# Kernel tuning notes

Hardware: AMD Instinct MI355X
Metric: run time of the kernel (lower is better)

Reference implementation:

```python
import jax, jax.numpy as jnp
import numpy as np
import math

D_MODEL = 1024
N_HEAD = 16
HEAD_DIM = D_MODEL // N_HEAD
SEQ_LEN = 512
INIT_SIZE = 1568  # from RelativeSinusoidalPositionalEmbedding default


def _rel_pos_embedding(seq_len, embedding_dim):
    # Replicates RelativeSinusoidalPositionalEmbedding with init_size=1568
    num_embeddings = INIT_SIZE + 1  # 1569
    half_dim = embedding_dim // 2
    scale = math.log(10000.0) / (half_dim - 1)
    freqs = np.exp(np.arange(half_dim, dtype=np.float32) * -scale)
    pos = np.arange(-(num_embeddings // 2), num_embeddings // 2, dtype=np.float32)  # [-785, 784)
    emb = pos[:, None] * freqs[None, :]
    weights = np.concatenate([np.sin(emb), np.cos(emb)], axis=1).astype(np.float32)  # (1569, d)
    weights[0, :] = 0.0  # padding_idx
    origin_shift = num_embeddings // 2 + 1  # 785
    positions = np.arange(-seq_len, seq_len) + origin_shift
    embed = weights[positions]  # (2*seq_len, d)
    return jnp.asarray(embed.T)  # (d, 2*seq_len), matching .T in __init__


def setup_inputs() -> dict:
    key = jax.random.key(0)
    k1, k2, k3, k4, k5 = jax.random.split(key, 5)
    x = jax.random.normal(k1, (8, SEQ_LEN, D_MODEL), dtype=jnp.float32)
    prev = jax.random.normal(k2, (8, N_HEAD, SEQ_LEN, SEQ_LEN), dtype=jnp.float32)
    # Linear(d_model, 3*d_model, bias=False): store as (d_model, 3*d_model) for x @ W
    Wqkv = jax.random.normal(k3, (D_MODEL, 3 * D_MODEL), dtype=jnp.float32) / math.sqrt(D_MODEL)
    r_r_bias = jax.random.normal(k4, (1, N_HEAD, 1, HEAD_DIM), dtype=jnp.float32) * 0.02
    r_w_bias = jax.random.normal(k5, (1, N_HEAD, 1, HEAD_DIM), dtype=jnp.float32) * 0.02
    rel_pos = _rel_pos_embedding(SEQ_LEN, HEAD_DIM)  # (head_dim, 2*seq_len)
    return {"x": x, "prev": prev, "Wqkv": Wqkv, "r_r_bias": r_r_bias,
            "r_w_bias": r_w_bias, "rel_pos": rel_pos, "skip_op": 1}


def _shift(BD, seq_len):
    # BD: (b, h, L, 2L) -> (b, h, L, L) via Transformer-XL pad/reshape trick
    b, h, L, two_L = BD.shape
    BD = jnp.pad(BD, ((0, 0), (0, 0), (0, 0), (0, 1)))        # (b,h,L,2L+1)
    BD = BD.reshape(b, h, -1, L)                               # (b,h,2L+1,L)
    BD = BD[:, :, :-1].reshape(b, h, L, -1)                    # (b,h,L,2L)
    return BD[:, :, :, seq_len:]                               # (b,h,L,L)


def reference(x, prev, Wqkv, r_r_bias, r_w_bias, rel_pos, skip_op):
    b, L, d = x.shape
    qkv = x @ Wqkv                                             # (b,L,3d)
    q, k, v = jnp.split(qkv, 3, axis=-1)
    q = q.reshape(b, L, N_HEAD, HEAD_DIM).transpose(0, 2, 1, 3)  # (b,h,L,hd)
    k = k.reshape(b, L, N_HEAD, HEAD_DIM).transpose(0, 2, 1, 3)
    v = v.reshape(b, L, N_HEAD, HEAD_DIM).transpose(0, 2, 1, 3)

    AC = jnp.einsum('bhqd,bhkd->bhqk', q + r_r_bias, k)
    BD = jnp.einsum('bhqd,dp->bhqp', q + r_w_bias, rel_pos)    # (b,h,L,2L)
    BD = _shift(BD, SEQ_LEN)
    E = jnp.einsum('bhkd,dp->bhkp', k, rel_pos)
    E = _shift(E, SEQ_LEN).transpose(0, 1, 3, 2)
    attn_score = (AC + BD + E) / math.sqrt(HEAD_DIM)
    if skip_op:
        attn_score = attn_score + prev
    prev_out = attn_score
    attn = jax.nn.softmax(attn_score, axis=-1)
    out = jnp.einsum('bhqk,bhkd->bhqd', attn, v)
    out = out.transpose(0, 2, 1, 3).reshape(b, L, d)
    return out, prev_out
```

## Files before the change

kernel.cpp:

```cpp
#include <hip/hip_runtime.h>
#include <hip/hip_bf16.h>
#include <math.h>

namespace {
constexpr int Bn = 8;
constexpr int Hn = 16;
constexpr int Ln = 512;
constexpr int HD = 64;
constexpr int DM = 1024;
constexpr int TL = 1024;
constexpr size_t QS  = (size_t)Bn * Hn * Ln * HD;
constexpr size_t FSz = (size_t)Hn * Ln * Ln;
constexpr size_t WN  = (size_t)DM * 3 * DM;
}

typedef __bf16 bf16x8 __attribute__((ext_vector_type(8)));
typedef float f32x4 __attribute__((ext_vector_type(4)));

typedef __attribute__((address_space(1))) void as1_void_t;
typedef __attribute__((address_space(3))) void as3_void_t;

__device__ __forceinline__ void gload_lds16(const void* g, void* l) {
  __builtin_amdgcn_global_load_lds((as1_void_t*)g, (as3_void_t*)l, 16, 0, 0);
}

__device__ __forceinline__ unsigned short f2bf(float f) {
  unsigned int u = __float_as_uint(f);
  u += 0x7fffu + ((u >> 16) & 1u);
  return (unsigned short)(u >> 16);
}
__device__ __forceinline__ float bf2f(unsigned short h) {
  return __uint_as_float(((unsigned int)h) << 16);
}

__global__ __launch_bounds__(256) void conv_x(const float* __restrict__ x,
                                              unsigned short* __restrict__ xh,
                                              unsigned short* __restrict__ xl) {
  size_t i = ((size_t)blockIdx.x * 256 + threadIdx.x) * 4;
  float4 v = *(const float4*)(x + i);
  unsigned short h0 = f2bf(v.x), h1 = f2bf(v.y), h2 = f2bf(v.z), h3 = f2bf(v.w);
  ushort4 hv = make_ushort4(h0, h1, h2, h3);
  ushort4 lv = make_ushort4(f2bf(v.x - bf2f(h0)), f2bf(v.y - bf2f(h1)),
                            f2bf(v.z - bf2f(h2)), f2bf(v.w - bf2f(h3)));
  *(ushort4*)(xh + i) = hv;
  *(ushort4*)(xl + i) = lv;
}

__global__ __launch_bounds__(256) void conv_w(const float* __restrict__ W,
                                              unsigned short* __restrict__ wh,
                                              unsigned short* __restrict__ wl) {
  __shared__ unsigned short Th[64][72];
  __shared__ unsigned short Tl[64][72];
  const int t = threadIdx.x;
  const int n0 = blockIdx.x * 64;
  const int k0 = blockIdx.y * 64;
#pragma unroll
  for (int i = 0; i < 4; ++i) {
    int row = i * 16 + (t >> 4);
    int col = (t & 15) * 4;
    float4 v = *(const float4*)(W + (size_t)(k0 + row) * 3072 + n0 + col);
    unsigned short h;
    h = f2bf(v.x); Th[row][col + 0] = h; Tl[row][col + 0] = f2bf(v.x - bf2f(h));
    h = f2bf(v.y); Th[row][col + 1] = h; Tl[row][col + 1] = f2bf(v.y - bf2f(h));
    h = f2bf(v.z); Th[row][col + 2] = h; Tl[row][col + 2] = f2bf(v.z - bf2f(h));
    h = f2bf(v.w); Th[row][col + 3] = h; Tl[row][col + 3] = f2bf(v.w - bf2f(h));
  }
  __syncthreads();
  const int rn = t & 63, qq = t >> 6;
  unsigned int hw[8], lw[8];
#pragma unroll
  for (int j = 0; j < 8; ++j) {
    unsigned short a = Th[qq * 16 + 2 * j][rn], b = Th[qq * 16 + 2 * j + 1][rn];
    hw[j] = (unsigned int)a | ((unsigned int)b << 16);
    unsigned short c = Tl[qq * 16 + 2 * j][rn], d = Tl[qq * 16 + 2 * j + 1][rn];
    lw[j] = (unsigned int)c | ((unsigned int)d << 16);
  }
  size_t o = (size_t)(n0 + rn) * 1024 + k0 + qq * 16;
  *(uint4*)(wh + o)     = make_uint4(hw[0], hw[1], hw[2], hw[3]);
  *(uint4*)(wh + o + 8) = make_uint4(hw[4], hw[5], hw[6], hw[7]);
  *(uint4*)(wl + o)     = make_uint4(lw[0], lw[1], lw[2], lw[3]);
  *(uint4*)(wl + o + 8) = make_uint4(lw[4], lw[5], lw[6], lw[7]);
}

__global__ __launch_bounds__(256, 2) void qkv_mfma(const unsigned short* __restrict__ xh,
                                                   const unsigned short* __restrict__ xl,
                                                   const unsigned short* __restrict__ wh,
                                                   const unsigned short* __restrict__ wl,
                                                   float* __restrict__ qarr,
                                                   float* __restrict__ karr,
                                                   float* __restrict__ varr) {
  __shared__ alignas(16) unsigned short Ah[128 * 32];
  __shared__ alignas(16) unsigned short Al[128 * 32];
  __shared__ alignas(16) unsigned short Bh[128 * 32];
  __shared__ alignas(16) unsigned short Bl[128 * 32];
  const int t = threadIdx.x;
  const int lane = t & 63;
  const int w = t >> 6;
  const int m0 = blockIdx.y * 128;
  const int n0 = blockIdx.x * 128;
  const int wr = w >> 1, wc = w & 1;
  const int l16 = lane & 15, s = lane >> 4;

  const unsigned short* gsrc = (w == 0) ? xh : (w == 1) ? xl : (w == 2) ? wh : wl;
  unsigned short* lbase = (w == 0) ? Ah : (w == 1) ? Al : (w == 2) ? Bh : Bl;
  const int rbase = (w < 2) ? m0 : n0;
  const int srow = lane >> 2, sc = lane & 3;

  int aoff[4], boff[4];
#pragma unroll
  for (int f = 0; f < 4; ++f) {
    int Rm = wr * 64 + f * 16 + l16;
    aoff[f] = Rm * 64 + ((s ^ ((Rm >> 1) & 3)) << 4);
    int Rn = wc * 64 + f * 16 + l16;
    boff[f] = Rn * 64 + ((s ^ ((Rn >> 1) & 3)) << 4);
  }

  f32x4 acc[4][4];
#pragma unroll
  for (int i = 0; i < 4; ++i)
#pragma unroll
    for (int j = 0; j < 4; ++j) acc[i][j] = (f32x4){0.f, 0.f, 0.f, 0.f};

  const char* Ahc = (const char*)Ah;
  const char* Alc = (const char*)Al;
  const char* Bhc = (const char*)Bh;
  const char* Blc = (const char*)Bl;

  for (int k0 = 0; k0 < 1024; k0 += 32) {
#pragma unroll
    for (int u = 0; u < 8; ++u) {
      int row = u * 16 + srow;
      int chunk = sc ^ ((row >> 1) & 3);
      gload_lds16(gsrc + (size_t)(rbase + row) * 1024 + k0 + chunk * 8,
                  lbase + u * 512);
    }
    __syncthreads();

    bf16x8 a_h[4], a_l[4], b_h[4], b_l[4];
#pragma unroll
    for (int f = 0; f < 4; ++f) {
      a_h[f] = *(const bf16x8*)(Ahc + aoff[f]);
      b_h[f] = *(const bf16x8*)(Bhc + boff[f]);
    }
#pragma unroll
    for (int i = 0; i < 4; ++i)
#pragma unroll
      for (int j = 0; j < 4; ++j)
        acc[i][j] = __builtin_amdgcn_mfma_f32_16x16x32_bf16(a_h[i], b_h[j], acc[i][j], 0, 0, 0);
#pragma unroll
    for (int f = 0; f < 4; ++f) b_l[f] = *(const bf16x8*)(Blc + boff[f]);
#pragma unroll
    for (int i = 0; i < 4; ++i)
#pragma unroll
      for (int j = 0; j < 4; ++j)
        acc[i][j] = __builtin_amdgcn_mfma_f32_16x16x32_bf16(a_h[i], b_l[j], acc[i][j], 0, 0, 0);
#pragma unroll
    for (int f = 0; f < 4; ++f) a_l[f] = *(const bf16x8*)(Alc + aoff[f]);
#pragma unroll
    for (int i = 0; i < 4; ++i)
#pragma unroll
      for (int j = 0; j < 4; ++j)
        acc[i][j] = __builtin_amdgcn_mfma_f32_16x16x32_bf16(a_l[i], b_h[j], acc[i][j], 0, 0, 0);
    __syncthreads();
  }

  const int part = n0 >> 10;
  float* dst = (part == 0) ? qarr : (part == 1 ? karr : varr);
  const int nb = n0 & 1023;
#pragma unroll
  for (int i = 0; i < 4; ++i) {
#pragma unroll
    for (int j = 0; j < 4; ++j) {
      const int n = nb + wc * 64 + j * 16 + l16;
      const int h = n >> 6, d = n & 63;
#pragma unroll
      for (int r = 0; r < 4; ++r) {
        int m = m0 + wr * 64 + i * 16 + (lane >> 4) * 4 + r;
        int bb = m >> 9, l = m & 511;
        dst[(((size_t)(bb * Hn + h) * Ln + l) << 6) + d] = acc[i][j][r];
      }
    }
  }
}

__global__ __launch_bounds__(256) void fg_gemm(const float* __restrict__ qarr,
                                               const float* __restrict__ karr,
                                               const float* __restrict__ rwb,
                                               const float* __restrict__ R,
                                               float* __restrict__ Fs,
                                               float* __restrict__ Gs,
                                               int b) {
  const int m0 = blockIdx.y * 64;
  const int n0 = blockIdx.x * 64;
  if (m0 + n0 + 126 < 512 || m0 + n0 >= 1024) return;

  __shared__ float As[64][68];
  __shared__ float Rs[64][68];
  const int t = threadIdx.x;
  const int h = blockIdx.z >> 1;
  const int which = blockIdx.z & 1;
  const float* A = (which == 0 ? qarr : karr) + (size_t)(b * Hn + h) * Ln * HD;

#pragma unroll
  for (int i = 0; i < 4; ++i) {
    int idx = t + i * 256;
    int r = idx >> 4;
    int c4 = (idx & 15) * 4;
    float4 av = *(const float4*)(A + (size_t)(m0 + r) * HD + c4);
    if (which == 0) {
      float4 bv = *(const float4*)(rwb + h * HD + c4);
      av.x += bv.x; av.y += bv.y; av.z += bv.z; av.w += bv.w;
    }
    As[c4 + 0][r] = av.x; As[c4 + 1][r] = av.y;
    As[c4 + 2][r] = av.z; As[c4 + 3][r] = av.w;
    *(float4*)(&Rs[r][c4]) = *(const float4*)(R + (size_t)r * TL + n0 + c4);
  }
  __syncthreads();
  const int tr = t >> 4, tc = t & 15;
  float acc[4][4];
#pragma unroll
  for (int i = 0; i < 4; ++i)
#pragma unroll
    for (int j = 0; j < 4; ++j) acc[i][j] = 0.f;
#pragma unroll 16
  for (int kk = 0; kk < 64; ++kk) {
    float a[4], bb[4];
    *(float4*)(a)  = *(const float4*)(&As[kk][tr * 4]);
    *(float4*)(bb) = *(const float4*)(&Rs[kk][tc * 4]);
#pragma unroll
    for (int i = 0; i < 4; ++i)
#pragma unroll
      for (int j = 0; j < 4; ++j) acc[i][j] = fmaf(a[i], bb[j], acc[i][j]);
  }
  if (which == 0) {
    float* O = Fs + (size_t)h * Ln * Ln;
#pragma unroll
    for (int i = 0; i < 4; ++i) {
      const int q = m0 + tr * 4 + i;
#pragma unroll
      for (int jj = 0; jj < 4; ++jj) {
        const int p = n0 + tc * 4 + jj;
        const int j = p + q - 512;
        if ((unsigned)j < 512u) O[((size_t)q << 9) + j] = acc[i][jj];
      }
    }
  } else {
    float* O = Gs + (size_t)h * Ln * Ln;
#pragma unroll
    for (int i = 0; i < 4; ++i) {
      const int jrow = m0 + tr * 4 + i;
#pragma unroll
      for (int jj = 0; jj < 4; ++jj) {
        const int p = n0 + tc * 4 + jj;
        const int q = p + jrow - 512;
        if ((unsigned)q < 512u) O[((size_t)q << 9) + jrow] = acc[i][jj];
      }
    }
  }
}

__global__ __launch_bounds__(256) void attn_fused(const float* __restrict__ qarr,
                                                  const float* __restrict__ karr,
                                                  const float* __restrict__ varr,
                                                  const float* __restrict__ rrb,
                                                  const float* __restrict__ Fs,
                                                  const float* __restrict__ Gs,
                                                  const float* __restrict__ prev,
                                                  const int* __restrict__ skip,
                                                  float* __restrict__ out,
                                                  float* __restrict__ pout,
                                                  int b) {
  __shared__ float qrT[64][18];
  __shared__ float ktT[64][68];
  __shared__ float vt[64][68];
  __shared__ float St[16][68];
  __shared__ float red[16][16];
  __shared__ float mrun[16], lrun[16], mnew_s[16], alpha_s[16];

  const int t = threadIdx.x;
  const int h = blockIdx.y;
  const int q0 = blockIdx.x * 16;
  const float pf = (skip[0] != 0) ? 1.f : 0.f;
  const size_t bh = (size_t)(b * Hn + h);

  {
    int r = t >> 4, c4 = (t & 15) * 4;
    float4 av = *(const float4*)(qarr + (bh * Ln + q0 + r) * HD + c4);
    float4 bv = *(const float4*)(rrb + h * HD + c4);
    qrT[c4 + 0][r] = av.x + bv.x; qrT[c4 + 1][r] = av.y + bv.y;
    qrT[c4 + 2][r] = av.z + bv.z; qrT[c4 + 3][r] = av.w + bv.w;
  }
  if (t < 16) { mrun[t] = -INFINITY; lrun[t] = 0.f; }

  const int tq = t >> 4, tj = t & 15;
  const int d = t & 63, qg = t >> 6;
  float O[4] = {0.f, 0.f, 0.f, 0.f};

  for (int jt = 0; jt < 8; ++jt) {
    const int j0 = jt * 64;
    __syncthreads();
#pragma unroll
    for (int i = 0; i < 4; ++i) {
      int idx = t + i * 256;
      int r = idx >> 4, c4 = (idx & 15) * 4;
      float4 kv = *(const float4*)(karr + (bh * Ln + j0 + r) * HD + c4);
      ktT[c4 + 0][r] = kv.x; ktT[c4 + 1][r] = kv.y;
      ktT[c4 + 2][r] = kv.z; ktT[c4 + 3][r] = kv.w;
      *(float4*)(&vt[r][c4]) = *(const float4*)(varr + (bh * Ln + j0 + r) * HD + c4);
    }
    __syncthreads();

    float s[4] = {0.f, 0.f, 0.f, 0.f};
#pragma unroll 8
    for (int dd = 0; dd < 64; ++dd) {
      float a = qrT[dd][tq];
      float4 bv = *(const float4*)(&ktT[dd][tj * 4]);
      s[0] = fmaf(a, bv.x, s[0]);
      s[1] = fmaf(a, bv.y, s[1]);
      s[2] = fmaf(a, bv.z, s[2]);
      s[3] = fmaf(a, bv.w, s[3]);
    }
    {
      const int q = q0 + tq;
      const size_t pbase = ((bh * Ln + q) << 9) + j0 + tj * 4;
      const size_t fbase = (((size_t)h * Ln + q) << 9) + j0 + tj * 4;
      float4 pv4 = *(const float4*)(prev + pbase);
      float4 fv4 = *(const float4*)(Fs + fbase);
      float4 gv4 = *(const float4*)(Gs + fbase);
      const float pin[4] = {pv4.x, pv4.y, pv4.z, pv4.w};
      const float fin[4] = {fv4.x, fv4.y, fv4.z, fv4.w};
      const float gin[4] = {gv4.x, gv4.y, gv4.z, gv4.w};
      float4 o4;
      float* o4p = &o4.x;
#pragma unroll
      for (int ji = 0; ji < 4; ++ji) {
        float sc = (s[ji] + fin[ji] + gin[ji]) * 0.125f + pf * pin[ji];
        o4p[ji] = sc;
        s[ji] = sc;
        St[tq][tj * 4 + ji] = sc;
      }
      *(float4*)(pout + pbase) = o4;
    }
    __syncthreads();
    {
      const int r = t >> 4, seg = t & 15;
      float mx = St[r][seg * 4];
#pragma unroll
      for (int u = 1; u < 4; ++u) mx = fmaxf(mx, St[r][seg * 4 + u]);
      red[r][seg] = mx;
    }
    __syncthreads();
    if (t < 16) {
      float mx = red[t][0];
#pragma unroll
      for (int u = 1; u < 16; ++u) mx = fmaxf(mx, red[t][u]);
      float mn = fmaxf(mrun[t], mx);
      alpha_s[t] = __expf(mrun[t] - mn);
      mnew_s[t] = mn;
      mrun[t] = mn;
    }
    __syncthreads();
    {
      const float mn = mnew_s[tq];
#pragma unroll
      for (int ji = 0; ji < 4; ++ji) St[tq][tj * 4 + ji] = __expf(s[ji] - mn);
    }
    __syncthreads();
    {
      const int r = t >> 4, seg = t & 15;
      float sm = 0.f;
#pragma unroll
      for (int u = 0; u < 4; ++u) sm += St[r][seg * 4 + u];
      red[r][seg] = sm;
    }
    __syncthreads();
    if (t < 16) {
      float sm = 0.f;
#pragma unroll
      for (int u = 0; u < 16; ++u) sm += red[t][u];
      lrun[t] = lrun[t] * alpha_s[t] + sm;
    }
#pragma unroll
    for (int i = 0; i < 4; ++i) O[i] *= alpha_s[qg * 4 + i];
#pragma unroll 8
    for (int j = 0; j < 64; ++j) {
      float vv = vt[j][d];
#pragma unroll
      for (int i = 0; i < 4; ++i) O[i] = fmaf(St[qg * 4 + i][j], vv, O[i]);
    }
  }
  __syncthreads();
#pragma unroll
  for (int i = 0; i < 4; ++i) {
    int lq = qg * 4 + i;
    float val = O[i] / lrun[lq];
    out[((size_t)b * Ln + q0 + lq) * DM + h * HD + d] = val;
  }
}

extern "C" void kernel_launch(void* const* d_in, const int* in_sizes, int n_in,
                              void* d_out, int out_size, void* d_ws, size_t ws_size,
                              hipStream_t stream) {
  const float* x    = (const float*)d_in[0];
  const float* prev = (const float*)d_in[1];
  const float* W    = (const float*)d_in[2];
  const float* rrb  = (const float*)d_in[3];
  const float* rwb  = (const float*)d_in[4];
  const float* R    = (const float*)d_in[5];
  const int*   skip = (const int*)d_in[6];

  float* out  = (float*)d_out;
  float* pout = out + (size_t)Bn * Ln * DM;

  float* ws = (float*)d_ws;
  float* qarr = ws;
  float* karr = ws + QS;
  float* varr = ws + 2 * QS;
  float* Farr = ws + 3 * QS;
  float* Garr = Farr + FSz;

  unsigned short* xh = (unsigned short*)Farr;
  unsigned short* xl = xh + QS;
  unsigned short* wh = xl + QS;
  unsigned short* wl = wh + WN;

  conv_x<<<dim3(4096), 256, 0, stream>>>(x, xh, xl);
  conv_w<<<dim3(48, 16), 256, 0, stream>>>(W, wh, wl);
  qkv_mfma<<<dim3(24, 32), 256, 0, stream>>>(xh, xl, wh, wl, qarr, karr, varr);
  for (int b = 0; b < Bn; ++b) {
    fg_gemm<<<dim3(TL / 64, Ln / 64, Hn * 2), 256, 0, stream>>>(qarr, karr, rwb, R, Farr, Garr, b);
    attn_fused<<<dim3(Ln / 16, Hn), 256, 0, stream>>>(qarr, karr, varr, rrb, Farr, Garr,
                                                      prev, skip, out, pout, b);
  }
}
```

Measured before the change: 1.056 ms.

## Move attention QK and PV products to split-bf16 MFMA with single-wave blocks

Replaces the scalar FP32 attention kernel with a one-wave MFMA kernel that computes QK^T and P·V using a three-term hi/lo bf16 split to keep near-FP32 accuracy. The QKV GEMM epilogue now also emits bf16 hi/lo copies of q+r_r_bias and k, plus a transposed V, so the attention kernel can load MFMA fragments directly. Softmax reductions move from shared memory with many barriers to wave shuffles. This trades extra workspace and epilogue stores, plus smaller 64-thread blocks, for far fewer scalar FMAs and no block-level syncs.

```diff
diff --git a/kernel.cpp b/kernel.cpp
--- a/kernel.cpp
+++ b/kernel.cpp
@@ -86,9 +86,15 @@
                                                    const unsigned short* __restrict__ xl,
                                                    const unsigned short* __restrict__ wh,
                                                    const unsigned short* __restrict__ wl,
+                                                   const float* __restrict__ rrb,
                                                    float* __restrict__ qarr,
                                                    float* __restrict__ karr,
-                                                   float* __restrict__ varr) {
+                                                   unsigned short* __restrict__ qrh,
+                                                   unsigned short* __restrict__ qrl,
+                                                   unsigned short* __restrict__ kharr,
+                                                   unsigned short* __restrict__ klarr,
+                                                   unsigned short* __restrict__ vTh,
+                                                   unsigned short* __restrict__ vTl) {
   __shared__ alignas(16) unsigned short Ah[128 * 32];
   __shared__ alignas(16) unsigned short Al[128 * 32];
   __shared__ alignas(16) unsigned short Bh[128 * 32];
@@ -165,7 +171,6 @@
   }
 
   const int part = n0 >> 10;
-  float* dst = (part == 0) ? qarr : (part == 1 ? karr : varr);
   const int nb = n0 & 1023;
 #pragma unroll
   for (int i = 0; i < 4; ++i) {
@@ -173,11 +178,45 @@
     for (int j = 0; j < 4; ++j) {
       const int n = nb + wc * 64 + j * 16 + l16;
       const int h = n >> 6, d = n & 63;
-#pragma unroll
-      for (int r = 0; r < 4; ++r) {
-        int m = m0 + wr * 64 + i * 16 + (lane >> 4) * 4 + r;
-        int bb = m >> 9, l = m & 511;
-        dst[(((size_t)(bb * Hn + h) * Ln + l) << 6) + d] = acc[i][j][r];
+      const int mb = m0 + wr * 64 + i * 16 + (lane >> 4) * 4;
+      const int bb = mb >> 9, lb = mb & 511;
+      const size_t rowbase = ((size_t)(bb * Hn + h) * Ln + lb) << 6;
+      if (part == 0) {
+        const float rr = rrb[h * HD + d];
+#pragma unroll
+        for (int r = 0; r < 4; ++r) {
+          const float v = acc[i][j][r];
+          const size_t qi = rowbase + ((size_t)r << 6) + d;
+          qarr[qi] = v;
+          const float qv = v + rr;
+          const unsigned short hh = f2bf(qv);
+          qrh[qi] = hh;
+          qrl[qi] = f2bf(qv - bf2f(hh));
+        }
+      } else if (part == 1) {
+#pragma unroll
+        for (int r = 0; r < 4; ++r) {
+          const float v = acc[i][j][r];
+          const size_t qi = rowbase + ((size_t)r << 6) + d;
+          karr[qi] = v;
+          const unsigned short hh = f2bf(v);
+          kharr[qi] = hh;
+          klarr[qi] = f2bf(v - bf2f(hh));
+        }
+      } else {
+        ushort4 hv, lv;
+        unsigned short* hp = &hv.x;
+        unsigned short* lp = &lv.x;
+#pragma unroll
+        for (int r = 0; r < 4; ++r) {
+          const float v = acc[i][j][r];
+          const unsigned short hh = f2bf(v);
+          hp[r] = hh;
+          lp[r] = f2bf(v - bf2f(hh));
+        }
+        const size_t vi = ((size_t)(bb * Hn + h) * HD + d) * Ln + lb;
+        *(ushort4*)(vTh + vi) = hv;
+        *(ushort4*)(vTl + vi) = lv;
       }
     }
   }
@@ -259,142 +298,150 @@
   }
 }
 
-__global__ __launch_bounds__(256) void attn_fused(const float* __restrict__ qarr,
-                                                  const float* __restrict__ karr,
-                                                  const float* __restrict__ varr,
-                                                  const float* __restrict__ rrb,
-                                                  const float* __restrict__ Fs,
-                                                  const float* __restrict__ Gs,
-                                                  const float* __restrict__ prev,
-                                                  const int* __restrict__ skip,
-                                                  float* __restrict__ out,
-                                                  float* __restrict__ pout,
-                                                  int b) {
-  __shared__ float qrT[64][18];
-  __shared__ float ktT[64][68];
-  __shared__ float vt[64][68];
-  __shared__ float St[16][68];
-  __shared__ float red[16][16];
-  __shared__ float mrun[16], lrun[16], mnew_s[16], alpha_s[16];
-
-  const int t = threadIdx.x;
+__global__ __launch_bounds__(64) void attn_mfma(const unsigned short* __restrict__ qrh,
+                                                const unsigned short* __restrict__ qrl,
+                                                const unsigned short* __restrict__ kharr,
+                                                const unsigned short* __restrict__ klarr,
+                                                const unsigned short* __restrict__ vTh,
+                                                const unsigned short* __restrict__ vTl,
+                                                const float* __restrict__ Fs,
+                                                const float* __restrict__ Gs,
+                                                const float* __restrict__ prev,
+                                                const int* __restrict__ skip,
+                                                float* __restrict__ out,
+                                                float* __restrict__ pout,
+                                                int b) {
+  __shared__ alignas(16) unsigned short PhL[16 * 64];
+  __shared__ alignas(16) unsigned short PlL[16 * 64];
+  const int lane = threadIdx.x & 63;
+  const int s = lane >> 4, l16 = lane & 15;
   const int h = blockIdx.y;
   const int q0 = blockIdx.x * 16;
+  const size_t bh = (size_t)(b * Hn + h);
   const float pf = (skip[0] != 0) ? 1.f : 0.f;
-  const size_t bh = (size_t)(b * Hn + h);
-
-  {
-    int r = t >> 4, c4 = (t & 15) * 4;
-    float4 av = *(const float4*)(qarr + (bh * Ln + q0 + r) * HD + c4);
-    float4 bv = *(const float4*)(rrb + h * HD + c4);
-    qrT[c4 + 0][r] = av.x + bv.x; qrT[c4 + 1][r] = av.y + bv.y;
-    qrT[c4 + 2][r] = av.z + bv.z; qrT[c4 + 3][r] = av.w + bv.w;
-  }
-  if (t < 16) { mrun[t] = -INFINITY; lrun[t] = 0.f; }
-
-  const int tq = t >> 4, tj = t & 15;
-  const int d = t & 63, qg = t >> 6;
-  float O[4] = {0.f, 0.f, 0.f, 0.f};
+
+  bf16x8 aqh[2], aql[2];
+#pragma unroll
+  for (int kd = 0; kd < 2; ++kd) {
+    const size_t a = ((bh * Ln + q0 + l16) << 6) + kd * 32 + s * 8;
+    aqh[kd] = *(const bf16x8*)(qrh + a);
+    aql[kd] = *(const bf16x8*)(qrl + a);
+  }
+
+  float m_run[4] = {-INFINITY, -INFINITY, -INFINITY, -INFINITY};
+  float l_run[4] = {0.f, 0.f, 0.f, 0.f};
+  f32x4 O[4];
+#pragma unroll
+  for (int fo = 0; fo < 4; ++fo) O[fo] = (f32x4){0.f, 0.f, 0.f, 0.f};
+
+  const int qrow = q0 + s * 4;
 
   for (int jt = 0; jt < 8; ++jt) {
     const int j0 = jt * 64;
-    __syncthreads();
-#pragma unroll
-    for (int i = 0; i < 4; ++i) {
-      int idx = t + i * 256;
-      int r = idx >> 4, c4 = (idx & 15) * 4;
-      float4 kv = *(const float4*)(karr + (bh * Ln + j0 + r) * HD + c4);
-      ktT[c4 + 0][r] = kv.x; ktT[c4 + 1][r] = kv.y;
-      ktT[c4 + 2][r] = kv.z; ktT[c4 + 3][r] = kv.w;
-      *(float4*)(&vt[r][c4]) = *(const float4*)(varr + (bh * Ln + j0 + r) * HD + c4);
-    }
-    __syncthreads();
-
-    float s[4] = {0.f, 0.f, 0.f, 0.f};
-#pragma unroll 8
-    for (int dd = 0; dd < 64; ++dd) {
-      float a = qrT[dd][tq];
-      float4 bv = *(const float4*)(&ktT[dd][tj * 4]);
-      s[0] = fmaf(a, bv.x, s[0]);
-      s[1] = fmaf(a, bv.y, s[1]);
-      s[2] = fmaf(a, bv.z, s[2]);
-      s[3] = fmaf(a, bv.w, s[3]);
-    }
-    {
-      const int q = q0 + tq;
-      const size_t pbase = ((bh * Ln + q) << 9) + j0 + tj * 4;
-      const size_t fbase = (((size_t)h * Ln + q) << 9) + j0 + tj * 4;
-      float4 pv4 = *(const float4*)(prev + pbase);
-      float4 fv4 = *(const float4*)(Fs + fbase);
-      float4 gv4 = *(const float4*)(Gs + fbase);
-      const float pin[4] = {pv4.x, pv4.y, pv4.z, pv4.w};
-      const float fin[4] = {fv4.x, fv4.y, fv4.z, fv4.w};
-      const float gin[4] = {gv4.x, gv4.y, gv4.z, gv4.w};
-      float4 o4;
-      float* o4p = &o4.x;
-#pragma unroll
-      for (int ji = 0; ji < 4; ++ji) {
-        float sc = (s[ji] + fin[ji] + gin[ji]) * 0.125f + pf * pin[ji];
-        o4p[ji] = sc;
-        s[ji] = sc;
-        St[tq][tj * 4 + ji] = sc;
-      }
-      *(float4*)(pout + pbase) = o4;
-    }
-    __syncthreads();
-    {
-      const int r = t >> 4, seg = t & 15;
-      float mx = St[r][seg * 4];
-#pragma unroll
-      for (int u = 1; u < 4; ++u) mx = fmaxf(mx, St[r][seg * 4 + u]);
-      red[r][seg] = mx;
-    }
-    __syncthreads();
-    if (t < 16) {
-      float mx = red[t][0];
-#pragma unroll
-      for (int u = 1; u < 16; ++u) mx = fmaxf(mx, red[t][u]);
-      float mn = fmaxf(mrun[t], mx);
-      alpha_s[t] = __expf(mrun[t] - mn);
-      mnew_s[t] = mn;
-      mrun[t] = mn;
-    }
-    __syncthreads();
-    {
-      const float mn = mnew_s[tq];
-#pragma unroll
-      for (int ji = 0; ji < 4; ++ji) St[tq][tj * 4 + ji] = __expf(s[ji] - mn);
-    }
-    __syncthreads();
-    {
-      const int r = t >> 4, seg = t & 15;
-      float sm = 0.f;
-#pragma unroll
-      for (int u = 0; u < 4; ++u) sm += St[r][seg * 4 + u];
-      red[r][seg] = sm;
-    }
-    __syncthreads();
-    if (t < 16) {
-      float sm = 0.f;
-#pragma unroll
-      for (int u = 0; u < 16; ++u) sm += red[t][u];
-      lrun[t] = lrun[t] * alpha_s[t] + sm;
-    }
-#pragma unroll
-    for (int i = 0; i < 4; ++i) O[i] *= alpha_s[qg * 4 + i];
-#pragma unroll 8
-    for (int j = 0; j < 64; ++j) {
-      float vv = vt[j][d];
-#pragma unroll
-      for (int i = 0; i < 4; ++i) O[i] = fmaf(St[qg * 4 + i][j], vv, O[i]);
-    }
-  }
-  __syncthreads();
-#pragma unroll
-  for (int i = 0; i < 4; ++i) {
-    int lq = qg * 4 + i;
-    float val = O[i] / lrun[lq];
-    out[((size_t)b * Ln + q0 + lq) * DM + h * HD + d] = val;
+
+    f32x4 S[4];
+#pragma unroll
+    for (int fi = 0; fi < 4; ++fi) S[fi] = (f32x4){0.f, 0.f, 0.f, 0.f};
+#pragma unroll
+    for (int kd = 0; kd < 2; ++kd) {
+#pragma unroll
+      for (int fi = 0; fi < 4; ++fi) {
+        const size_t ka = ((bh * Ln + j0 + fi * 16 + l16) << 6) + kd * 32 + s * 8;
+        const bf16x8 bkh = *(const bf16x8*)(kharr + ka);
+        const bf16x8 bkl = *(const bf16x8*)(klarr + ka);
+        S[fi] = __builtin_amdgcn_mfma_f32_16x16x32_bf16(aqh[kd], bkh, S[fi], 0, 0, 0);
+        S[fi] = __builtin_amdgcn_mfma_f32_16x16x32_bf16(aqh[kd], bkl, S[fi], 0, 0, 0);
+        S[fi] = __builtin_amdgcn_mfma_f32_16x16x32_bf16(aql[kd], bkh, S[fi], 0, 0, 0);
+      }
+    }
+
+    float sc[4][4];
+    float mx[4] = {-INFINITY, -INFINITY, -INFINITY, -INFINITY};
+#pragma unroll
+    for (int fi = 0; fi < 4; ++fi) {
+      const int j = j0 + fi * 16 + l16;
+#pragma unroll
+      for (int r = 0; r < 4; ++r) {
+        const int q = qrow + r;
+        const size_t fb = (((size_t)h * Ln + q) << 9) + j;
+        const size_t pb = ((bh * Ln + q) << 9) + j;
+        const float v = (S[fi][r] + Fs[fb] + Gs[fb]) * 0.125f + pf * prev[pb];
+        pout[pb] = v;
+        sc[fi][r] = v;
+        mx[r] = fmaxf(mx[r], v);
+      }
+    }
+
+    float al[4];
+#pragma unroll
+    for (int r = 0; r < 4; ++r) {
+      float m = mx[r];
+      m = fmaxf(m, __shfl_xor(m, 1));
+      m = fmaxf(m, __shfl_xor(m, 2));
+      m = fmaxf(m, __shfl_xor(m, 4));
+      m = fmaxf(m, __shfl_xor(m, 8));
+      const float mn = fmaxf(m_run[r], m);
+      al[r] = __expf(m_run[r] - mn);
+      m_run[r] = mn;
+    }
+
+    float sum[4] = {0.f, 0.f, 0.f, 0.f};
+#pragma unroll
+    for (int fi = 0; fi < 4; ++fi) {
+      const int jloc = fi * 16 + l16;
+      const int chunk = jloc >> 3, sub = jloc & 7;
+#pragma unroll
+      for (int r = 0; r < 4; ++r) {
+        const float p = __expf(sc[fi][r] - m_run[r]);
+        sum[r] += p;
+        const unsigned short ph = f2bf(p);
+        const unsigned short pl = f2bf(p - bf2f(ph));
+        const int qloc = s * 4 + r;
+        const int idx = (qloc << 6) + ((chunk ^ (qloc & 7)) << 3) + sub;
+        PhL[idx] = ph;
+        PlL[idx] = pl;
+      }
+    }
+#pragma unroll
+    for (int r = 0; r < 4; ++r) {
+      float sm = sum[r];
+      sm += __shfl_xor(sm, 1);
+      sm += __shfl_xor(sm, 2);
+      sm += __shfl_xor(sm, 4);
+      sm += __shfl_xor(sm, 8);
+      l_run[r] = l_run[r] * al[r] + sm;
+    }
+
+#pragma unroll
+    for (int fo = 0; fo < 4; ++fo)
+#pragma unroll
+      for (int r = 0; r < 4; ++r) O[fo][r] *= al[r];
+
+#pragma unroll
+    for (int kj = 0; kj < 2; ++kj) {
+      const int raddr = (l16 << 6) + (((kj * 4 + s) ^ (l16 & 7)) << 3);
+      const bf16x8 pah = *(const bf16x8*)(PhL + raddr);
+      const bf16x8 pal = *(const bf16x8*)(PlL + raddr);
+#pragma unroll
+      for (int fo = 0; fo < 4; ++fo) {
+        const size_t va = ((bh << 6) + fo * 16 + l16) * (size_t)Ln + j0 + kj * 32 + s * 8;
+        const bf16x8 vbh = *(const bf16x8*)(vTh + va);
+        const bf16x8 vbl = *(const bf16x8*)(vTl + va);
+        O[fo] = __builtin_amdgcn_mfma_f32_16x16x32_bf16(pah, vbh, O[fo], 0, 0, 0);
+        O[fo] = __builtin_amdgcn_mfma_f32_16x16x32_bf16(pah, vbl, O[fo], 0, 0, 0);
+        O[fo] = __builtin_amdgcn_mfma_f32_16x16x32_bf16(pal, vbh, O[fo], 0, 0, 0);
+      }
+    }
+  }
+
+#pragma unroll
+  for (int r = 0; r < 4; ++r) {
+    const float inv = 1.0f / l_run[r];
+    const size_t ob = ((size_t)b * Ln + qrow + r) * DM + h * HD;
+#pragma unroll
+    for (int fo = 0; fo < 4; ++fo) {
+      out[ob + fo * 16 + l16] = O[fo][r] * inv;
+    }
   }
 }
 
@@ -415,21 +462,27 @@
   float* ws = (float*)d_ws;
   float* qarr = ws;
   float* karr = ws + QS;
-  float* varr = ws + 2 * QS;
-  float* Farr = ws + 3 * QS;
+  unsigned short* qrh = (unsigned short*)(ws + 2 * QS);
+  unsigned short* qrl = qrh + QS;
+  unsigned short* kh  = qrl + QS;
+  unsigned short* kl  = kh + QS;
+  unsigned short* vTh = kl + QS;
+  unsigned short* vTl = vTh + QS;
+  float* Farr = ws + 5 * QS;
   float* Garr = Farr + FSz;
 
   unsigned short* xh = (unsigned short*)Farr;
   unsigned short* xl = xh + QS;
-  unsigned short* wh = xl + QS;
-  unsigned short* wl = wh + WN;
+  unsigned short* wwh = xl + QS;
+  unsigned short* wwl = wwh + WN;
 
   conv_x<<<dim3(4096), 256, 0, stream>>>(x, xh, xl);
-  conv_w<<<dim3(48, 16), 256, 0, stream>>>(W, wh, wl);
-  qkv_mfma<<<dim3(24, 32), 256, 0, stream>>>(xh, xl, wh, wl, qarr, karr, varr);
+  conv_w<<<dim3(48, 16), 256, 0, stream>>>(W, wwh, wwl);
+  qkv_mfma<<<dim3(24, 32), 256, 0, stream>>>(xh, xl, wwh, wwl, rrb, qarr, karr,
+                                             qrh, qrl, kh, kl, vTh, vTl);
   for (int b = 0; b < Bn; ++b) {
     fg_gemm<<<dim3(TL / 64, Ln / 64, Hn * 2), 256, 0, stream>>>(qarr, karr, rwb, R, Farr, Garr, b);
-    attn_fused<<<dim3(Ln / 16, Hn), 256, 0, stream>>>(qarr, karr, varr, rrb, Farr, Garr,
-                                                      prev, skip, out, pout, b);
-  }
-}
+    attn_mfma<<<dim3(Ln / 16, Hn), 64, 0, stream>>>(qrh, qrl, kh, kl, vTh, vTl,
+                                                    Farr, Garr, prev, skip, out, pout, b);
+  }
+}
```

Result: slower. 1.118 ms (+5.9%).
